# Kernel optimization log

Measured on AMD Instinct MI355X. Metric: run time of the kernel, lower is better.

The kernel has to match this reference:

```python
import jax, jax.numpy as jnp
import numpy as np
import math

N_TERMS = 10
TWO_PI = 2.0 * math.pi


def _zernike_tables(n_terms):
    # Terms in the exact order of the torch loops: n in [0,n_terms), m in range(-n, n+1, 2).
    terms = []
    for n in range(n_terms):
        for m in range(-n, n + 1, 2):
            terms.append((n, m))
    T = len(terms)  # n_terms*(n_terms+1)/2 = 55 for n_terms=10
    C = np.zeros((T, n_terms), dtype=np.float32)  # C[t, p] = coeff of rho**p for term t
    ms = np.zeros(T, dtype=np.float32)
    for t, (n, m) in enumerate(terms):
        am = abs(m)
        for k in range((n - am) // 2 + 1):
            c = ((-1) ** k) * math.factorial(n - k) / (
                math.factorial(k)
                * math.factorial((n + am) // 2 - k)
                * math.factorial((n - am) // 2 - k)
            )
            C[t, n - 2 * k] += c
        ms[t] = m
    return C, ms


_C_NP, _MS_NP = _zernike_tables(N_TERMS)


def setup_inputs() -> dict:
    key = jax.random.key(0)
    x = jax.random.normal(key, (32, 1, 1024, 1024), dtype=jnp.float32)
    return {"x": x}


def reference(x) -> jnp.ndarray:
    # FFT features
    fft_image = jnp.fft.rfft2(x)                    # [B,1,H,Wr], Wr = W//2+1
    magnitude = jnp.abs(fft_image)
    phase = jnp.angle(fft_image)
    pu = jnp.where(phase < 0, phase + TWO_PI, phase)  # "unwrapped" phase

    # Phase gradients (torch.gradient semantics == jnp.gradient: central diff, one-sided edges)
    grad_y, grad_x = jnp.gradient(pu, axis=(2, 3))

    # Zernike coefficients over the phase map grid
    B, _, H, Wr = pu.shape
    yv = jnp.linspace(-1.0, 1.0, H)
    xv = jnp.linspace(-1.0, 1.0, Wr)
    gy, gx = jnp.meshgrid(yv, xv, indexing="ij")   # [H,Wr]
    rho = jnp.sqrt(gx ** 2 + gy ** 2)
    theta = jnp.arctan2(gy, gx)
    mask = (rho <= 1.0).astype(pu.dtype)

    C = jnp.asarray(_C_NP)                          # [T,P]
    ms = jnp.asarray(_MS_NP)                        # [T]
    powers = jnp.arange(N_TERMS, dtype=pu.dtype)    # rho**0 .. rho**(n_terms-1)
    rho_pows = rho[None] ** powers[:, None, None]   # [P,H,Wr]
    R = jnp.einsum("tp,phw->thw", C, rho_pows)     # radial polynomials, [T,H,Wr]
    mt = ms[:, None, None] * theta[None]
    ang = jnp.where(ms[:, None, None] >= 0, jnp.cos(mt), jnp.sin(-mt))
    Z = R * ang                                     # [T,H,Wr]

    pm = pu[:, 0] * mask                            # [B,H,Wr]
    coeffs = jnp.einsum("bhw,thw->bt", pm, Z) / jnp.sum(mask)  # [B,T]

    # Slope stats (torch .std is unbiased -> ddof=1)
    slope_stats = jnp.concatenate(
        [
            grad_x.mean(axis=(2, 3)),
            grad_y.mean(axis=(2, 3)),
            grad_x.std(axis=(2, 3), ddof=1),
            grad_y.std(axis=(2, 3), ddof=1),
        ],
        axis=1,
    )                                               # [B,4]

    freq_features = jnp.max(magnitude, axis=(2, 3))  # [B,1]

    return jnp.concatenate([coeffs, slope_stats, freq_features], axis=1)  # [B,60]
```

## Files before the change

kernel.cpp:

```cpp
#include <hip/hip_runtime.h>
#include <math.h>

#define BATCH 32
#define HH 1024
#define WW 1024
#define WR 513
#define NPIX (HH * WR)
#define TWO_PI_F 6.28318530717958647692f

#define LGKM_SYNC() __asm__ __volatile__("s_waitcnt lgkmcnt(0)" ::: "memory")

__device__ __forceinline__ float2 cadd(float2 a, float2 b) { return make_float2(a.x + b.x, a.y + b.y); }
__device__ __forceinline__ float2 csub(float2 a, float2 b) { return make_float2(a.x - b.x, a.y - b.y); }
__device__ __forceinline__ float2 cmul(float2 a, float2 b) {
    return make_float2(a.x * b.x - a.y * b.y, a.x * b.y + a.y * b.x);
}

__device__ __forceinline__ float fast_atan2f(float y, float x) {
    float ax = __builtin_fabsf(x), ay = __builtin_fabsf(y);
    float mx = fmaxf(ax, ay), mn = fminf(ax, ay);
    float a = mn * __builtin_amdgcn_rcpf(mx);
    float s = a * a;
    float r = fmaf(fmaf(fmaf(fmaf(0.0208351f, s, -0.085133f), s, 0.180141f),
                        s, -0.3302995f), s, 0.999866f) * a;
    if (ay > ax) r = 1.5707963268f - r;
    if (x < 0.0f) r = 3.1415926536f - r;
    return (y < 0.0f) ? -r : r;
}

__device__ __forceinline__ constexpr int ridx(int k) { return ((k & 3) << 2) | (k >> 2); }

__device__ __forceinline__ void fft16_ip(float2* d) {
    const float2 Wt1[4] = {{1.f, 0.f},
                           {0.92387953f, -0.38268343f},
                           {0.70710678f, -0.70710678f},
                           {0.38268343f, -0.92387953f}};
    const float2 Wt2[4] = {{1.f, 0.f},
                           {0.70710678f, -0.70710678f},
                           {0.f, -1.f},
                           {-0.70710678f, -0.70710678f}};
    const float2 Wt3[4] = {{1.f, 0.f},
                           {0.38268343f, -0.92387953f},
                           {-0.70710678f, -0.70710678f},
                           {-0.92387953f, 0.38268343f}};
#pragma unroll
    for (int t = 0; t < 4; ++t) {
        float2 x0 = d[t], x1 = d[t + 4], x2 = d[t + 8], x3 = d[t + 12];
        float2 a0 = cadd(x0, x2), a1 = csub(x0, x2), a2 = cadd(x1, x3), a3 = csub(x1, x3);
        d[t]      = cadd(a0, a2);
        d[t + 4]  = cmul(make_float2(a1.x + a3.y, a1.y - a3.x), Wt1[t]);
        d[t + 8]  = cmul(csub(a0, a2), Wt2[t]);
        d[t + 12] = cmul(make_float2(a1.x - a3.y, a1.y + a3.x), Wt3[t]);
    }
#pragma unroll
    for (int r = 0; r < 4; ++r) {
        float2 x0 = d[4 * r], x1 = d[4 * r + 1], x2 = d[4 * r + 2], x3 = d[4 * r + 3];
        float2 e0 = cadd(x0, x2), e1 = csub(x0, x2), e2 = cadd(x1, x3), e3 = csub(x1, x3);
        d[4 * r]     = cadd(e0, e2);
        d[4 * r + 1] = make_float2(e1.x + e3.y, e1.y - e3.x);
        d[4 * r + 2] = csub(e0, e2);
        d[4 * r + 3] = make_float2(e1.x - e3.y, e1.y + e3.x);
    }
}

__device__ __forceinline__ void twiddle_tree(float2 T, float2* Wt) {
    Wt[1] = T;
    Wt[2] = cmul(T, T);
    Wt[3] = cmul(Wt[2], T);
    Wt[4] = cmul(Wt[2], Wt[2]);
    Wt[5] = cmul(Wt[4], Wt[1]);
    Wt[6] = cmul(Wt[4], Wt[2]);
    Wt[7] = cmul(Wt[4], Wt[3]);
    Wt[8] = cmul(Wt[4], Wt[4]);
    Wt[9]  = cmul(Wt[8], Wt[1]);
    Wt[10] = cmul(Wt[8], Wt[2]);
    Wt[11] = cmul(Wt[8], Wt[3]);
    Wt[12] = cmul(Wt[8], Wt[4]);
    Wt[13] = cmul(Wt[8], Wt[5]);
    Wt[14] = cmul(Wt[8], Wt[6]);
    Wt[15] = cmul(Wt[8], Wt[7]);
}

__device__ __forceinline__ void wave_fft1024(float2* v, float2* sb, int lane) {
    fft16_ip(v);
    float s, c;
    __sincosf(-TWO_PI_F * (float)lane * (1.0f / 1024.0f), &s, &c);
    float2 Wt[16];
    twiddle_tree(make_float2(c, s), Wt);
#pragma unroll
    for (int k2 = 1; k2 < 16; ++k2) v[ridx(k2)] = cmul(v[ridx(k2)], Wt[k2]);
    const int k2p = lane & 15, qp = lane >> 4;
#pragma unroll
    for (int k2 = 0; k2 < 16; ++k2) sb[(k2 << 6) | (lane ^ k2)] = v[ridx(k2)];
    LGKM_SYNC();
#pragma unroll
    for (int m = 0; m < 16; ++m) v[m] = sb[(k2p << 6) | ((4 * m + qp) ^ k2p)];
    LGKM_SYNC();
    fft16_ip(v);
    __sincosf(-TWO_PI_F * (float)qp * (1.0f / 64.0f), &s, &c);
    twiddle_tree(make_float2(c, s), Wt);
#pragma unroll
    for (int km = 1; km < 16; ++km) v[ridx(km)] = cmul(v[ridx(km)], Wt[km]);
    const bool hi2 = (lane & 32) != 0, hi1 = (lane & 16) != 0;
#pragma unroll
    for (int m = 0; m < 16; ++m) {
        float2 a = v[m];
        float2 o = make_float2(__shfl_xor(a.x, 32, 64), __shfl_xor(a.y, 32, 64));
        float2 s1 = hi2 ? csub(o, a) : cadd(a, o);
        if (hi2 && hi1) s1 = make_float2(s1.y, -s1.x);
        float2 o2 = make_float2(__shfl_xor(s1.x, 16, 64), __shfl_xor(s1.y, 16, 64));
        v[m] = hi1 ? csub(o2, s1) : cadd(s1, o2);
    }
}

__global__ __launch_bounds__(256, 4) void row_fft_kernel(const float* __restrict__ x,
                                                         float2* __restrict__ rf2) {
    __shared__ float2 buf[4][1024];
    const int t = threadIdx.x, w = t >> 6, lane = t & 63;
    const int b = blockIdx.x >> 7;
    const int h0 = (blockIdx.x & 127) * 8;
    const float* r0 = x + ((long long)b * HH + h0 + 2 * w) * (long long)WW;
    const float* r1 = r0 + WW;
    float2 v[16];
#pragma unroll
    for (int j = 0; j < 16; ++j) v[j] = make_float2(r0[lane + 64 * j], r1[lane + 64 * j]);
    float2* mybuf = &buf[w][0];
    wave_fft1024(v, mybuf, lane);
    const int kq = 2 * ((lane >> 4) & 1) + ((lane >> 5) & 1);
    const int kbase = (lane & 15) + 256 * kq;
#pragma unroll
    for (int m = 0; m < 16; ++m) mybuf[kbase + 16 * m] = v[ridx(m)];
    __syncthreads();
    for (int idx = t; idx < 513 * 8; idx += 256) {
        int k = idx >> 3, j = idx & 7, p = j >> 1, which = j & 1;
        float2 zk = buf[p][k];
        float2 zn = buf[p][(1024 - k) & 1023];
        float2 val = which ? make_float2(0.5f * (zk.y + zn.y), 0.5f * (zn.x - zk.x))
                           : make_float2(0.5f * (zk.x + zn.x), 0.5f * (zk.y - zn.y));
        rf2[((long long)b * WR + k) * 1024 + h0 + j] = val;
    }
}

__device__ __forceinline__ constexpr int brev5(int k) {
    return ((k & 1) << 4) | ((k & 2) << 2) | (k & 4) | ((k & 8) >> 2) | ((k & 16) >> 4);
}

__device__ __forceinline__ void fft32_dif(float2* d) {
    const float2 TW[16] = {
        {1.f, 0.f},
        {0.98078528f, -0.19509032f},
        {0.92387953f, -0.38268343f},
        {0.83146961f, -0.55557023f},
        {0.70710678f, -0.70710678f},
        {0.55557023f, -0.83146961f},
        {0.38268343f, -0.92387953f},
        {0.19509032f, -0.98078528f},
        {0.f, -1.f},
        {-0.19509032f, -0.98078528f},
        {-0.38268343f, -0.92387953f},
        {-0.55557023f, -0.83146961f},
        {-0.70710678f, -0.70710678f},
        {-0.83146961f, -0.55557023f},
        {-0.92387953f, -0.38268343f},
        {-0.98078528f, -0.19509032f}};
#pragma unroll
    for (int s = 0; s < 5; ++s) {
        const int h = 16 >> s;
#pragma unroll
        for (int b = 0; b < 32; b += 2 * h) {
#pragma unroll
            for (int j = 0; j < h; ++j) {
                float2 a = d[b + j], c = d[b + j + h];
                d[b + j]     = cadd(a, c);
                d[b + j + h] = cmul(csub(a, c), TW[j << s]);
            }
        }
    }
}

#define ZPIX(VV, YVV)                                                          \
    {                                                                          \
        const float yv_ = (YVV);                                               \
        const float r2_ = xv2 + yv_ * yv_;                                     \
        if (r2_ <= 1.0f) {                                                     \
            cnt += 1.0f;                                                       \
            const float rho = sqrtf(r2_);                                      \
            const float inv = rsqrtf(r2_);                                     \
            const float c1 = xv * inv;                                         \
            const float s1 = yv_ * inv;                                        \
            const float c2 = 2.f * c1 * c1 - 1.f;                              \
            const float c3 = 2.f * c1 * c2 - c1;                               \
            const float c4 = 2.f * c1 * c3 - c2;                               \
            const float c5 = 2.f * c1 * c4 - c3;                               \
            const float c6 = 2.f * c1 * c5 - c4;                               \
            const float c7 = 2.f * c1 * c6 - c5;                               \
            const float c8 = 2.f * c1 * c7 - c6;                               \
            const float c9 = 2.f * c1 * c8 - c7;                               \
            const float s2 = 2.f * c1 * s1;                                    \
            const float s3 = 2.f * c1 * s2 - s1;                               \
            const float s4 = 2.f * c1 * s3 - s2;                               \
            const float s5 = 2.f * c1 * s4 - s3;                               \
            const float s6 = 2.f * c1 * s5 - s4;                               \
            const float s7 = 2.f * c1 * s6 - s5;                               \
            const float s8 = 2.f * c1 * s7 - s6;                               \
            const float s9 = 2.f * c1 * s8 - s7;                               \
            const float w0 = (VV), w1 = w0 * rho, w2 = w1 * rho, w3 = w2 * rho,\
                        w4 = w3 * rho, w5 = w4 * rho, w6 = w5 * rho,           \
                        w7 = w6 * rho, w8 = w7 * rho, w9 = w8 * rho;           \
            a00 += w0;                                                         \
            a11 += w1 * c1;                                                    \
            a20 += w2;      a22 += w2 * c2;                                    \
            a31 += w3 * c1; a33 += w3 * c3;                                    \
            a40 += w4;      a42 += w4 * c2; a44 += w4 * c4;                    \
            a51 += w5 * c1; a53 += w5 * c3; a55 += w5 * c5;                    \
            a60 += w6;      a62 += w6 * c2; a64 += w6 * c4; a66 += w6 * c6;    \
            a71 += w7 * c1; a73 += w7 * c3; a75 += w7 * c5; a77 += w7 * c7;    \
            a80 += w8;      a82 += w8 * c2; a84 += w8 * c4; a86 += w8 * c6;    \
            a88 += w8 * c8;                                                    \
            a91 += w9 * c1; a93 += w9 * c3; a95 += w9 * c5; a97 += w9 * c7;    \
            a99 += w9 * c9;                                                    \
            b11 += w1 * s1;                                                    \
            b22 += w2 * s2;                                                    \
            b31 += w3 * s1; b33 += w3 * s3;                                    \
            b42 += w4 * s2; b44 += w4 * s4;                                    \
            b51 += w5 * s1; b53 += w5 * s3; b55 += w5 * s5;                    \
            b62 += w6 * s2; b64 += w6 * s4; b66 += w6 * s6;                    \
            b71 += w7 * s1; b73 += w7 * s3; b75 += w7 * s5; b77 += w7 * s7;    \
            b82 += w8 * s2; b84 += w8 * s4; b86 += w8 * s6; b88 += w8 * s8;    \
            b91 += w9 * s1; b93 += w9 * s3; b95 += w9 * s5; b97 += w9 * s7;    \
            b99 += w9 * s9;                                                    \
        }                                                                      \
    }

#define WRED(var, idx)                                                     \
    {                                                                      \
        float r_ = var;                                                    \
        _Pragma("unroll")                                                  \
        for (int off_ = 32; off_; off_ >>= 1) r_ += __shfl_down(r_, off_); \
        if (lane == 0) red[w * 64 + (idx)] = r_;                           \
    }

__global__ __launch_bounds__(256, 2) void fused_col_stats_kernel(float2* __restrict__ rf2,
                                                                 float* __restrict__ magmax) {
    __shared__ float2 sb[8][1024];
    float* red = (float*)&sb[0][512];
    const int tid = threadIdx.x, w = tid >> 6, lane = tid & 63;
    const int n1 = lane & 31, s = lane >> 5;
    const int slot = 2 * w + s;
    const int bx = blockIdx.x, b = blockIdx.y;
    const int k0 = bx * 6;
    int kf = k0 - 1 + slot;
    kf = kf < 0 ? 0 : (kf > WR - 1 ? WR - 1 : kf);
    const float2* src = rf2 + ((long long)b * WR + kf) * 1024;

    float2 d[32];
#pragma unroll
    for (int j = 0; j < 32; ++j) d[j] = src[n1 + 32 * j];
    fft32_dif(d);
    float s0, c0;
    __sincosf(-TWO_PI_F * (float)n1 * (1.0f / 1024.0f), &s0, &c0);
    const float2 Tn = make_float2(c0, s0);
    float2 ww = Tn;
#pragma unroll
    for (int k1 = 1; k1 < 32; ++k1) {
        d[brev5(k1)] = cmul(d[brev5(k1)], ww);
        if (k1 < 31) ww = cmul(ww, Tn);
    }
    float2* myLDS = &sb[slot][0];
#pragma unroll
    for (int k1 = 0; k1 < 32; ++k1) myLDS[(k1 << 5) | (n1 ^ k1)] = d[brev5(k1)];
    LGKM_SYNC();
#pragma unroll
    for (int j = 0; j < 32; ++j) d[j] = myLDS[(n1 << 5) | (j ^ n1)];
    fft32_dif(d);

    float* pul_own = (float*)&sb[slot][0];
    float mmax = 0.0f;
#pragma unroll
    for (int k2 = 0; k2 < 32; ++k2) {
        float2 z = d[brev5(k2)];
        mmax = fmaxf(mmax, __builtin_amdgcn_sqrtf(z.x * z.x + z.y * z.y));
        float ph = fast_atan2f(z.y, z.x);
        pul_own[32 * k2 + n1] = (ph < 0.0f) ? ph + TWO_PI_F : ph;
    }
#pragma unroll
    for (int off = 16; off; off >>= 1) mmax = fmaxf(mmax, __shfl_xor(mmax, off, 64));
    if (n1 == 0) atomicMax((int*)(magmax + b), __float_as_int(mmax));
    __syncthreads();

    float a00 = 0.f, a11 = 0.f, a20 = 0.f, a22 = 0.f, a31 = 0.f, a33 = 0.f,
          a40 = 0.f, a42 = 0.f, a44 = 0.f, a51 = 0.f, a53 = 0.f, a55 = 0.f,
          a60 = 0.f, a62 = 0.f, a64 = 0.f, a66 = 0.f, a71 = 0.f, a73 = 0.f,
          a75 = 0.f, a77 = 0.f, a80 = 0.f, a82 = 0.f, a84 = 0.f, a86 = 0.f,
          a88 = 0.f, a91 = 0.f, a93 = 0.f, a95 = 0.f, a97 = 0.f, a99 = 0.f;
    float b11 = 0.f, b22 = 0.f, b31 = 0.f, b33 = 0.f, b42 = 0.f, b44 = 0.f,
          b51 = 0.f, b53 = 0.f, b55 = 0.f, b62 = 0.f, b64 = 0.f, b66 = 0.f,
          b71 = 0.f, b73 = 0.f, b75 = 0.f, b77 = 0.f, b82 = 0.f, b84 = 0.f,
          b86 = 0.f, b88 = 0.f, b91 = 0.f, b93 = 0.f, b95 = 0.f, b97 = 0.f,
          b99 = 0.f;
    float sgx = 0.f, sgx2 = 0.f, sgy = 0.f, sgy2 = 0.f, cnt = 0.f;

    for (int sl = 1; sl <= 6; ++sl) {
        const int k = k0 + sl - 1;
        if (k > WR - 1) break;
        const float xv = -1.0f + (1.0f / 256.0f) * (float)k;
        const float xv2 = xv * xv;
        const float* pc = (const float*)&sb[sl][0];
        const float* pm = (const float*)&sb[sl - 1][0];
        const float* pp = (const float*)&sb[sl + 1][0];
        for (int h = tid; h < 1024; h += 256) {
            const float v = pc[h];
            float gx, gy;
            if (k == 0)            gx = pp[h] - v;
            else if (k == WR - 1)  gx = v - pm[h];
            else                   gx = 0.5f * (pp[h] - pm[h]);
            if (h == 0)            gy = pc[1] - v;
            else if (h == 1023)    gy = v - pc[1022];
            else                   gy = 0.5f * (pc[h + 1] - pc[h - 1]);
            sgx += gx; sgx2 += gx * gx; sgy += gy; sgy2 += gy * gy;
            const float yv = -1.0f + (2.0f / 1023.0f) * (float)h;
            ZPIX(v, yv);
        }
    }

    WRED(a00, 0);  WRED(a11, 1);  WRED(a20, 2);  WRED(a22, 3);  WRED(a31, 4);
    WRED(a33, 5);  WRED(a40, 6);  WRED(a42, 7);  WRED(a44, 8);  WRED(a51, 9);
    WRED(a53, 10); WRED(a55, 11); WRED(a60, 12); WRED(a62, 13); WRED(a64, 14);
    WRED(a66, 15); WRED(a71, 16); WRED(a73, 17); WRED(a75, 18); WRED(a77, 19);
    WRED(a80, 20); WRED(a82, 21); WRED(a84, 22); WRED(a86, 23); WRED(a88, 24);
    WRED(a91, 25); WRED(a93, 26); WRED(a95, 27); WRED(a97, 28); WRED(a99, 29);
    WRED(b11, 30); WRED(b22, 31); WRED(b31, 32); WRED(b33, 33); WRED(b42, 34);
    WRED(b44, 35); WRED(b51, 36); WRED(b53, 37); WRED(b55, 38); WRED(b62, 39);
    WRED(b64, 40); WRED(b66, 41); WRED(b71, 42); WRED(b73, 43); WRED(b75, 44);
    WRED(b77, 45); WRED(b82, 46); WRED(b84, 47); WRED(b86, 48); WRED(b88, 49);
    WRED(b91, 50); WRED(b93, 51); WRED(b95, 52); WRED(b97, 53); WRED(b99, 54);
    WRED(sgx, 55); WRED(sgx2, 56); WRED(sgy, 57); WRED(sgy2, 58); WRED(cnt, 59);
    __syncthreads();
    if (tid < 60) {
        float sum = red[tid] + red[64 + tid] + red[128 + tid] + red[192 + tid];
        float* pdst = (float*)(rf2 + ((long long)b * WR + k0 + 2) * 1024);
        pdst[tid] = sum;
    }
}

__device__ int moment_index(int p, int a, int is_cos) {
    int ai = 0;
    for (int pp = 0; pp < 10; ++pp)
        for (int aa = (pp & 1); aa <= pp; aa += 2) {
            if (is_cos && pp == p && aa == a) return ai;
            ++ai;
        }
    for (int pp = 1; pp < 10; ++pp)
        for (int aa = ((pp & 1) ? 1 : 2); aa <= pp; aa += 2) {
            if (!is_cos && pp == p && aa == a) return ai;
            ++ai;
        }
    return 0;
}

__device__ float factf(int n) {
    float f = 1.0f;
    for (int i = 2; i <= n; ++i) f *= (float)i;
    return f;
}

__global__ void finalize_kernel(const float* __restrict__ rf2f,
                                const float* __restrict__ magmax,
                                float* __restrict__ out) {
    __shared__ float abf[64];
    const int b = blockIdx.x;
    const int j = threadIdx.x;
    if (j < 60) {
        float s = 0.0f;
        for (int i = 0; i < 86; ++i)
            s += rf2f[((long long)b * WR + 6 * i + 2) * 2048 + j];
        abf[j] = s;
    }
    __syncthreads();
    if (j >= 60) return;
    const float NF = (float)NPIX;
    float val;
    if (j < 55) {
        int tt = j, n = 0;
        while (tt >= n + 1) { tt -= (n + 1); ++n; }
        int m = -n + 2 * tt;
        int am = m < 0 ? -m : m;
        float s = 0.0f;
        for (int k = 0; k <= (n - am) / 2; ++k) {
            float c = factf(n - k) /
                      (factf(k) * factf((n + am) / 2 - k) * factf((n - am) / 2 - k));
            if (k & 1) c = -c;
            int p = n - 2 * k;
            s += c * abf[moment_index(p, am, m >= 0 ? 1 : 0)];
        }
        val = s / abf[59];
    } else if (j == 55) {
        val = abf[55] / NF;
    } else if (j == 56) {
        val = abf[57] / NF;
    } else if (j == 57) {
        float sum = abf[55], sq = abf[56];
        val = sqrtf(fmaxf(0.0f, (sq - sum * sum / NF) / (NF - 1.0f)));
    } else if (j == 58) {
        float sum = abf[57], sq = abf[58];
        val = sqrtf(fmaxf(0.0f, (sq - sum * sum / NF) / (NF - 1.0f)));
    } else {
        val = magmax[b];
    }
    out[b * 60 + j] = val;
}

extern "C" void kernel_launch(void* const* d_in, const int* in_sizes, int n_in,
                              void* d_out, int out_size, void* d_ws, size_t ws_size,
                              hipStream_t stream) {
    (void)in_sizes; (void)n_in; (void)out_size; (void)ws_size;
    const float* x = (const float*)d_in[0];
    float* out = (float*)d_out;

    float* magmax = (float*)d_ws;
    float2* rf2 = (float2*)((char*)d_ws + 16384);

    hipMemsetAsync(d_ws, 0, 16384, stream);
    row_fft_kernel<<<BATCH * 128, 256, 0, stream>>>(x, rf2);
    dim3 gridF(86, BATCH);
    fused_col_stats_kernel<<<gridF, 256, 0, stream>>>(rf2, magmax);
    finalize_kernel<<<BATCH, 64, 0, stream>>>((const float*)rf2, magmax, out);
}
```

Before: 442.6 us.

## Halve LDS footprint with split real/imag transpose and vectorize stats loop

```diff
diff --git a/kernel.cpp b/kernel.cpp
--- a/kernel.cpp
+++ b/kernel.cpp
@@ -240,10 +240,10 @@
         if (lane == 0) red[w * 64 + (idx)] = r_;                           \
     }
 
-__global__ __launch_bounds__(256, 2) void fused_col_stats_kernel(float2* __restrict__ rf2,
+__global__ __launch_bounds__(256, 4) void fused_col_stats_kernel(float2* __restrict__ rf2,
                                                                  float* __restrict__ magmax) {
-    __shared__ float2 sb[8][1024];
-    float* red = (float*)&sb[0][512];
+    __shared__ float sb[8][1024];
+    __shared__ float red[256];
     const int tid = threadIdx.x, w = tid >> 6, lane = tid & 63;
     const int n1 = lane & 31, s = lane >> 5;
     const int slot = 2 * w + s;
@@ -266,22 +266,28 @@
         d[brev5(k1)] = cmul(d[brev5(k1)], ww);
         if (k1 < 31) ww = cmul(ww, Tn);
     }
-    float2* myLDS = &sb[slot][0];
-#pragma unroll
-    for (int k1 = 0; k1 < 32; ++k1) myLDS[(k1 << 5) | (n1 ^ k1)] = d[brev5(k1)];
+    float* scr = &sb[slot][0];
+#pragma unroll
+    for (int k1 = 0; k1 < 32; ++k1) scr[(k1 << 5) | (n1 ^ k1)] = d[brev5(k1)].x;
     LGKM_SYNC();
-#pragma unroll
-    for (int j = 0; j < 32; ++j) d[j] = myLDS[(n1 << 5) | (j ^ n1)];
+    float tx[32];
+#pragma unroll
+    for (int j = 0; j < 32; ++j) tx[j] = scr[(n1 << 5) | (j ^ n1)];
+    LGKM_SYNC();
+#pragma unroll
+    for (int k1 = 0; k1 < 32; ++k1) scr[(k1 << 5) | (n1 ^ k1)] = d[brev5(k1)].y;
+    LGKM_SYNC();
+#pragma unroll
+    for (int j = 0; j < 32; ++j) d[j] = make_float2(tx[j], scr[(n1 << 5) | (j ^ n1)]);
     fft32_dif(d);
 
-    float* pul_own = (float*)&sb[slot][0];
     float mmax = 0.0f;
 #pragma unroll
     for (int k2 = 0; k2 < 32; ++k2) {
         float2 z = d[brev5(k2)];
         mmax = fmaxf(mmax, __builtin_amdgcn_sqrtf(z.x * z.x + z.y * z.y));
         float ph = fast_atan2f(z.y, z.x);
-        pul_own[32 * k2 + n1] = (ph < 0.0f) ? ph + TWO_PI_F : ph;
+        scr[32 * k2 + n1] = (ph < 0.0f) ? ph + TWO_PI_F : ph;
     }
 #pragma unroll
     for (int off = 16; off; off >>= 1) mmax = fmaxf(mmax, __shfl_xor(mmax, off, 64));
@@ -300,27 +306,48 @@
           b99 = 0.f;
     float sgx = 0.f, sgx2 = 0.f, sgy = 0.f, sgy2 = 0.f, cnt = 0.f;
 
+    const int h4 = tid * 4;
+    const float ystep = 2.0f / 1023.0f;
+    const float yv0 = -1.0f + ystep * (float)h4;
+
     for (int sl = 1; sl <= 6; ++sl) {
         const int k = k0 + sl - 1;
         if (k > WR - 1) break;
         const float xv = -1.0f + (1.0f / 256.0f) * (float)k;
         const float xv2 = xv * xv;
-        const float* pc = (const float*)&sb[sl][0];
-        const float* pm = (const float*)&sb[sl - 1][0];
-        const float* pp = (const float*)&sb[sl + 1][0];
-        for (int h = tid; h < 1024; h += 256) {
-            const float v = pc[h];
-            float gx, gy;
-            if (k == 0)            gx = pp[h] - v;
-            else if (k == WR - 1)  gx = v - pm[h];
-            else                   gx = 0.5f * (pp[h] - pm[h]);
-            if (h == 0)            gy = pc[1] - v;
-            else if (h == 1023)    gy = v - pc[1022];
-            else                   gy = 0.5f * (pc[h + 1] - pc[h - 1]);
-            sgx += gx; sgx2 += gx * gx; sgy += gy; sgy2 += gy * gy;
-            const float yv = -1.0f + (2.0f / 1023.0f) * (float)h;
-            ZPIX(v, yv);
+        const float* pc = &sb[sl][0];
+        const float* pm = &sb[sl - 1][0];
+        const float* pp = &sb[sl + 1][0];
+        const float4 vc = *reinterpret_cast<const float4*>(pc + h4);
+        float4 gx4;
+        if (k == 0) {
+            const float4 vp = *reinterpret_cast<const float4*>(pp + h4);
+            gx4 = make_float4(vp.x - vc.x, vp.y - vc.y, vp.z - vc.z, vp.w - vc.w);
+        } else if (k == WR - 1) {
+            const float4 vm = *reinterpret_cast<const float4*>(pm + h4);
+            gx4 = make_float4(vc.x - vm.x, vc.y - vm.y, vc.z - vm.z, vc.w - vm.w);
+        } else {
+            const float4 vm = *reinterpret_cast<const float4*>(pm + h4);
+            const float4 vp = *reinterpret_cast<const float4*>(pp + h4);
+            gx4 = make_float4(0.5f * (vp.x - vm.x), 0.5f * (vp.y - vm.y),
+                              0.5f * (vp.z - vm.z), 0.5f * (vp.w - vm.w));
         }
+        const float left  = pc[h4 > 0 ? h4 - 1 : 0];
+        const float right = pc[h4 < 1020 ? h4 + 4 : 1023];
+        const float gy0 = (h4 == 0)    ? vc.y - vc.x : 0.5f * (vc.y - left);
+        const float gy1 = 0.5f * (vc.z - vc.x);
+        const float gy2 = 0.5f * (vc.w - vc.y);
+        const float gy3 = (h4 == 1020) ? vc.w - vc.z : 0.5f * (right - vc.z);
+
+        sgx  += gx4.x + gx4.y + gx4.z + gx4.w;
+        sgx2 += gx4.x * gx4.x + gx4.y * gx4.y + gx4.z * gx4.z + gx4.w * gx4.w;
+        sgy  += gy0 + gy1 + gy2 + gy3;
+        sgy2 += gy0 * gy0 + gy1 * gy1 + gy2 * gy2 + gy3 * gy3;
+
+        ZPIX(vc.x, yv0);
+        ZPIX(vc.y, yv0 + ystep);
+        ZPIX(vc.z, yv0 + 2.0f * ystep);
+        ZPIX(vc.w, yv0 + 3.0f * ystep);
     }
 
     WRED(a00, 0);  WRED(a11, 1);  WRED(a20, 2);  WRED(a22, 3);  WRED(a31, 4);
```

After: 419.5 us. 1.06x faster.
